# Kernel optimization log

Measured on AMD Instinct MI355X. Metric: run time of the kernel, lower is better.

Reference implementation:

```python
import jax, jax.numpy as jnp
import numpy as np

# hyperparameters (from init_kwargs / repo defaults)
AMP_COEF = 1.0
ARG_COEF = 1.0
SSIM_COEF = 1.0
BETA = 1.0
STFT_COEF = 1e-4
EPS = 1e-8
STFT_F = 12
STFT_S = 4


def _gauss_kernel(size=11, sigma=1.5):
    x = jnp.arange(size, dtype=jnp.float32) - (size - 1) / 2.0
    g = jnp.exp(-0.5 * (x / sigma) ** 2)
    k = jnp.outer(g, g)
    return k / jnp.sum(k)


def _depthwise_filter(img, k):
    # img: [B,H,W,C]; 11x11 gaussian, VALID padding, depthwise (per-channel)
    c = img.shape[-1]
    kern = jnp.tile(k[:, :, None, None], (1, 1, 1, c))  # HWIO, I=1, O=C
    return jax.lax.conv_general_dilated(
        img, kern, (1, 1), 'VALID',
        dimension_numbers=('NHWC', 'HWIO', 'NHWC'),
        feature_group_count=c)


def ssim(x, y, max_val=1.0):
    # faithful to tf.image.ssim defaults: filter 11, sigma 1.5, k1=0.01, k2=0.03
    c1 = (0.01 * max_val) ** 2
    c2 = (0.03 * max_val) ** 2
    k = _gauss_kernel()
    mu_x = _depthwise_filter(x, k)
    mu_y = _depthwise_filter(y, k)
    var_x = _depthwise_filter(x * x, k) - mu_x * mu_x
    var_y = _depthwise_filter(y * y, k) - mu_y * mu_y
    cov = _depthwise_filter(x * y, k) - mu_x * mu_y
    lum = (2.0 * mu_x * mu_y + c1) / (mu_x * mu_x + mu_y * mu_y + c1)
    cs = (2.0 * cov + c2) / (var_x + var_y + c2)
    return jnp.mean(lum * cs, axis=(1, 2, 3))  # [B]


def stft(image, f=STFT_F, s=STFT_S):
    # image: [B,N,N,C] -> batched patchwise 2D FFT, cropped to [:f//2,:f//2]
    n = image.shape[1]
    p = (n - f) // s + 1          # num_conv per axis
    half = f // 2
    rows = (jnp.arange(p) * s)[:, None] + jnp.arange(f)   # [P, f]
    patches = image[:, rows]                              # [B,P,f,N,C]
    patches = patches[:, :, :, rows]                      # [B,P,f,P,f,C]
    patches = jnp.transpose(patches, (0, 1, 3, 2, 4, 5))  # [B,Pi,Pj,f,f,C]
    b, c = image.shape[0], image.shape[-1]
    patches = patches.reshape(b, p * p, f, f, c)          # k = i*P + j ordering
    fft = jnp.fft.fft2(patches.astype(jnp.complex64), axes=(2, 3))
    return fft[:, :, :half, :half, :]                     # [B,P*P,half,half,C]


def _freq_filter(f=STFT_F):
    lin = jnp.linspace(0.0, 1.0, f // 2)[:, None]
    return (lin * lin.T)[:, :, None]                      # [half,half,1]


def setup_inputs() -> dict:
    key = jax.random.key(0)
    k1, k2, k3, k4 = jax.random.split(key, 4)
    B, N, C, L = 32, 160, 3, 128
    return {
        'mean': jax.random.normal(k1, (B, L), dtype=jnp.float32),
        'logvar': jax.random.normal(k2, (B, L), dtype=jnp.float32),
        'x_in': jax.random.uniform(k3, (B, N, N, C), dtype=jnp.float32),
        'x_out': jax.random.uniform(k4, (B, N, N, C), dtype=jnp.float32),
    }


def reference(mean, logvar, x_in, x_out):
    # KLD per sample
    var = jnp.exp(logvar)
    kld = -0.5 * jnp.sum(1.0 + logvar - var - mean * mean, axis=1)  # [B]
    # SSIM recon term
    recons = SSIM_COEF * ssim(x_in, x_out, 1.0)                     # [B]
    # patchwise STFT amp/phase loss ('ours')
    stft_out = stft(x_out, STFT_F, STFT_S)
    stft_in = stft(x_in, STFT_F, STFT_S)
    ff = _freq_filter(STFT_F)                                       # [half,half,1]
    arg_diff = jnp.abs(jnp.angle(stft_out + EPS) - jnp.angle(stft_in + EPS))
    amp_diff = jnp.abs(jnp.abs(stft_out) - jnp.abs(stft_in))
    arg_loss = jnp.sum(arg_diff * ff, axis=(1, 2, 3, 4))            # [B]
    amp_loss = jnp.sum(amp_diff * ff, axis=(1, 2, 3, 4))            # [B]
    stft_loss = ARG_COEF * arg_loss + AMP_COEF * amp_loss
    loss = jnp.mean(BETA * kld + recons + STFT_COEF * stft_loss)
    return loss
```

## Files before the change

kernel.cpp:

```cpp
#include <hip/hip_runtime.h>
#include <hip/hip_fp16.h>
#include <math.h>

#define BATCH 32
#define NPIX 160
#define LDIM 128
#define OUT_SZ 150

#define THREADS 512
#define N_BLOCKS 1825
#define SCRATCH_OFF 2880
#define VSTRIDE 1296
#define SMEM_FLOATS 9360

__device__ constexpr float TWC[12] = { 1.f, 0.86602540f, 0.5f, 0.f, -0.5f, -0.86602540f,
                                      -1.f,-0.86602540f,-0.5f, 0.f,  0.5f,  0.86602540f};
__device__ constexpr float TWS[12] = { 0.f,-0.5f,-0.86602540f,-1.f,-0.86602540f,-0.5f,
                                       0.f, 0.5f, 0.86602540f, 1.f, 0.86602540f, 0.5f};

__device__ constexpr float GW[11] = {0.00102838f, 0.00759876f, 0.03600076f, 0.10936070f,
                                     0.21300554f, 0.26601172f, 0.21300554f, 0.10936070f,
                                     0.03600076f, 0.00759876f, 0.00102838f};

__device__ __forceinline__ float fast_atan2f(float y, float x) {
    float ax = fabsf(x), ay = fabsf(y);
    float mx = fmaxf(ax, ay), mn = fminf(ax, ay);
    float z = mn / mx;
    float z2 = z * z;
    float p = fmaf(z2, -0.01172120f, 0.05265332f);
    p = fmaf(z2, p, -0.11643287f);
    p = fmaf(z2, p, 0.19354346f);
    p = fmaf(z2, p, -0.33262347f);
    p = fmaf(z2, p, 0.99997726f);
    p = p * z;
    if (ay > ax) p = 1.57079632679489662f - p;
    if (x < 0.f) p = 3.14159265358979323f - p;
    return (y < 0.f) ? -p : p;
}

__device__ __forceinline__ float4 extract_c(float4 f0, float4 f1, float4 f2, int c) {
    if (c == 0) return make_float4(f0.x, f0.w, f1.z, f2.y);
    if (c == 1) return make_float4(f0.y, f1.x, f1.w, f2.z);
    return make_float4(f0.z, f1.y, f2.x, f2.w);
}

__global__ __launch_bounds__(THREADS) void work_kernel(const float* __restrict__ xin,
                                                       const float* __restrict__ xout,
                                                       const float* __restrict__ mean,
                                                       const float* __restrict__ logvar,
                                                       float* __restrict__ out) {
    __shared__ __align__(16) float SMEM[SMEM_FLOATS];
    __shared__ float sm8[8];
    const int tid = threadIdx.x;
    const int gid = blockIdx.x;
    float acc = 0.f;

    if (gid == 1824) {
        float a = 0.f;
        for (int i = tid; i < BATCH * LDIM; i += THREADS) {
            float m = mean[i], lv = logvar[i];
            a += -0.5f * (1.f + lv - expf(lv) - m * m) * (1.f / 32.f);
        }
        #pragma unroll
        for (int o = 32; o > 0; o >>= 1) a += __shfl_down(a, o, 64);
        if ((tid & 63) == 0) sm8[tid >> 6] = a;
        __syncthreads();
        if (tid == 0) {
            float s = sm8[0];
            #pragma unroll
            for (int i = 1; i < 8; ++i) s += sm8[i];
            atomicAdd(out, s);
        }
        return;
    }

    int b    = gid / 57;
    int rem  = gid % 57;
    int c    = rem / 19;
    int tile = rem % 19;
    int r0 = tile * 8;
    __half2* HXY = (__half2*)SMEM;
    __half2* RD  = (__half2*)(SMEM + SCRATCH_OFF);

    for (int t = tid; t < 720; t += THREADS) {
        int rr = t / 40;
        int cq = t % 40;
        int row = r0 + rr;
        float4 xa = make_float4(0.f, 0.f, 0.f, 0.f);
        float4 xb = make_float4(0.f, 0.f, 0.f, 0.f);
        if (row < NPIX) {
            size_t off = ((size_t)(b * 160 + row) * 160 + cq * 4) * 3;
            const float4* qa = (const float4*)(xin + off);
            const float4* qb = (const float4*)(xout + off);
            float4 a0 = qa[0], a1 = qa[1], a2 = qa[2];
            float4 b0 = qb[0], b1 = qb[1], b2 = qb[2];
            xa = extract_c(a0, a1, a2, c);
            xb = extract_c(b0, b1, b2, c);
        }
        __half2 h[4] __attribute__((aligned(16)));
        h[0] = __floats2half2_rn(xa.x, xb.x);
        h[1] = __floats2half2_rn(xa.y, xb.y);
        h[2] = __floats2half2_rn(xa.z, xb.z);
        h[3] = __floats2half2_rn(xa.w, xb.w);
        *(float4*)&HXY[rr * 160 + cq * 4] = *(float4*)h;
    }
    __syncthreads();

    for (int t = tid; t < 608; t += THREADS) {
        int pc = t % 38;
        int r  = t / 38;
        float4 raw[3];
        raw[0] = *(const float4*)&HXY[r * 160 + pc * 4];
        raw[1] = *(const float4*)&HXY[r * 160 + pc * 4 + 4];
        raw[2] = *(const float4*)&HXY[r * 160 + pc * 4 + 8];
        const __half2* hp = (const __half2*)raw;
        float xa[12], xb[12];
        #pragma unroll
        for (int j = 0; j < 12; ++j) {
            float2 xy = __half22float2(hp[j]);
            xa[j] = xy.x; xb[j] = xy.y;
        }
        #pragma unroll
        for (int img = 0; img < 2; ++img) {
            const float* x = img ? xb : xa;
            float ev[5] = {x[1]+x[11], x[2]+x[10], x[3]+x[9], x[4]+x[8], x[5]+x[7]};
            float ov[5] = {x[1]-x[11], x[2]-x[10], x[3]-x[9], x[4]-x[8], x[5]-x[7]};
            #pragma unroll
            for (int vv = 0; vv < 5; ++vv) {
                int v = vv + 1;
                float re = x[0] + ((v & 1) ? -x[6] : x[6]);
                float im = 0.f;
                #pragma unroll
                for (int j = 1; j <= 5; ++j) {
                    int kk = (v * j) % 12;
                    re = fmaf(ev[j-1], TWC[kk], re);
                    im = fmaf(ov[j-1], TWS[kk], im);
                }
                RD[((r * 5 + vv) * 2 + img) * 38 + pc] = __floats2half2_rn(re, im);
            }
        }
    }
    __syncthreads();

    if (tid < 380) {
        int pc = tid % 38;
        int vv = (tid / 38) % 5;
        int g  = tid / 190;
        float FR0[5] = {0,0,0,0,0}, FI0[5] = {0,0,0,0,0};
        float FR1[5] = {0,0,0,0,0}, FI1[5] = {0,0,0,0,0};
        #pragma unroll
        for (int i = 0; i < 6; ++i) {
            int rlo = 4 * g + i, rhi = rlo + 6;
            float2 a0 = __half22float2(RD[((rlo * 5 + vv) * 2 + 0) * 38 + pc]);
            float2 a6 = __half22float2(RD[((rhi * 5 + vv) * 2 + 0) * 38 + pc]);
            float2 b0 = __half22float2(RD[((rlo * 5 + vv) * 2 + 1) * 38 + pc]);
            float2 b6 = __half22float2(RD[((rhi * 5 + vv) * 2 + 1) * 38 + pc]);
            float spR0 = a0.x + a6.x, spI0 = a0.y + a6.y;
            float smR0 = a0.x - a6.x, smI0 = a0.y - a6.y;
            float spR1 = b0.x + b6.x, spI1 = b0.y + b6.y;
            float smR1 = b0.x - b6.x, smI1 = b0.y - b6.y;
            #pragma unroll
            for (int uu = 0; uu < 5; ++uu) {
                int u = uu + 1;
                int kk = (u * i) % 12;
                float cu = TWC[kk], su = TWS[kk];
                float sR0 = (u & 1) ? smR0 : spR0, sI0 = (u & 1) ? smI0 : spI0;
                float sR1 = (u & 1) ? smR1 : spR1, sI1 = (u & 1) ? smI1 : spI1;
                FR0[uu] = fmaf(cu, sR0, fmaf(-su, sI0, FR0[uu]));
                FI0[uu] = fmaf(cu, sI0, fmaf( su, sR0, FI0[uu]));
                FR1[uu] = fmaf(cu, sR1, fmaf(-su, sI1, FR1[uu]));
                FI1[uu] = fmaf(cu, sI1, fmaf( su, sR1, FI1[uu]));
            }
        }
        float sacc = 0.f;
        #pragma unroll
        for (int uu = 0; uu < 5; ++uu) {
            float aI = fast_atan2f(FI0[uu], FR0[uu] + 1e-8f);
            float aO = fast_atan2f(FI1[uu], FR1[uu] + 1e-8f);
            float mI = sqrtf(FR0[uu] * FR0[uu] + FI0[uu] * FI0[uu]);
            float mO = sqrtf(FR1[uu] * FR1[uu] + FI1[uu] * FI1[uu]);
            float ff = (float)((uu + 1) * (vv + 1)) * 0.04f;
            sacc += ff * (fabsf(aO - aI) + fabsf(mO - mI));
        }
        acc += sacc * (1e-4f / 32.f);
    }
    __syncthreads();

    for (int t = tid; t < 320; t += THREADS) {
        int orow = t / 40;
        int cbase = (t % 40) * 4;
        float ax[4] = {0,0,0,0}, ay[4] = {0,0,0,0};
        float axx[4] = {0,0,0,0}, ayy[4] = {0,0,0,0}, axy[4] = {0,0,0,0};
        #pragma unroll
        for (int kk = 0; kk < 11; ++kk) {
            float4 raw = *(const float4*)&HXY[(orow + kk) * 160 + cbase];
            const __half2* hp = (const __half2*)&raw;
            float wg = GW[kk];
            #pragma unroll
            for (int o = 0; o < 4; ++o) {
                float2 xy = __half22float2(hp[o]);
                ax[o]  += wg * xy.x;          ay[o]  += wg * xy.y;
                axx[o] += wg * (xy.x * xy.x); ayy[o] += wg * (xy.y * xy.y);
                axy[o] += wg * (xy.x * xy.y);
            }
        }
        int base = SCRATCH_OFF + orow * 160 + cbase;
        *(float4*)&SMEM[base + 0 * VSTRIDE] = make_float4(ax[0],  ax[1],  ax[2],  ax[3]);
        *(float4*)&SMEM[base + 1 * VSTRIDE] = make_float4(ay[0],  ay[1],  ay[2],  ay[3]);
        *(float4*)&SMEM[base + 2 * VSTRIDE] = make_float4(axx[0], axx[1], axx[2], axx[3]);
        *(float4*)&SMEM[base + 3 * VSTRIDE] = make_float4(ayy[0], ayy[1], ayy[2], ayy[3]);
        *(float4*)&SMEM[base + 4 * VSTRIDE] = make_float4(axy[0], axy[1], axy[2], axy[3]);
    }
    __syncthreads();

    {
        float hacc = 0.f;
        for (int t = tid; t < 600; t += THREADS) {
            int orow = t / 75;
            int oc = (t % 75) * 2;
            float st[5][2];
            #pragma unroll
            for (int p = 0; p < 5; ++p) {
                float vals[12];
                #pragma unroll
                for (int kk = 0; kk < 12; ++kk)
                    vals[kk] = SMEM[SCRATCH_OFF + p * VSTRIDE + orow * 160 + oc + kk];
                float s0 = 0.f, s1 = 0.f;
                #pragma unroll
                for (int kk = 0; kk < 11; ++kk) {
                    s0 += GW[kk] * vals[kk];
                    s1 += GW[kk] * vals[kk + 1];
                }
                st[p][0] = s0; st[p][1] = s1;
            }
            const float c1 = 1e-4f, c2 = 9e-4f;
            if (r0 + orow < OUT_SZ) {
                #pragma unroll
                for (int o = 0; o < 2; ++o) {
                    float mx = st[0][o], my = st[1][o];
                    float vx = st[2][o] - mx * mx;
                    float vy = st[3][o] - my * my;
                    float cv = st[4][o] - mx * my;
                    float lum = (2.f * mx * my + c1) / (mx * mx + my * my + c1);
                    float cs  = (2.f * cv + c2) / (vx + vy + c2);
                    hacc += lum * cs;
                }
            }
        }
        acc += hacc * (1.f / (32.f * 150.f * 150.f * 3.f));
    }

    #pragma unroll
    for (int o = 32; o > 0; o >>= 1) acc += __shfl_down(acc, o, 64);
    if ((tid & 63) == 0) sm8[tid >> 6] = acc;
    __syncthreads();
    if (tid == 0) {
        float s = sm8[0];
        #pragma unroll
        for (int i = 1; i < 8; ++i) s += sm8[i];
        atomicAdd(out, s);
    }
}

extern "C" void kernel_launch(void* const* d_in, const int* in_sizes, int n_in,
                              void* d_out, int out_size, void* d_ws, size_t ws_size,
                              hipStream_t stream) {
    const float* mean   = (const float*)d_in[0];
    const float* logvar = (const float*)d_in[1];
    const float* xin    = (const float*)d_in[2];
    const float* xout   = (const float*)d_in[3];
    float* out = (float*)d_out;

    hipMemsetAsync(out, 0, sizeof(float), stream);
    work_kernel<<<N_BLOCKS, THREADS, 0, stream>>>(xin, xout, mean, logvar, out);
}
```

Measured before the change: 122.6 us.

## Use packed half2 math for STFT and SSIM filters, fast rcp/sqrt

Moves the row/column DFT and the SSIM separable Gaussian filtering from fp32 to packed __half2 arithmetic, so x and y channels are processed together in one instruction. The intermediate scratch layout shrinks: mu and E[x^2] are stored as half2 and only the cross term stays fp32, with padded row strides. Divisions become hardware reciprocal and sqrt builtins. This cuts ALU and LDS traffic, but fp16 accumulation of variance and FFT terms risks precision loss, especially in the SSIM variance subtraction.

```diff
diff --git a/kernel.cpp b/kernel.cpp
--- a/kernel.cpp
+++ b/kernel.cpp
@@ -9,9 +9,12 @@
 
 #define THREADS 512
 #define N_BLOCKS 1825
-#define SCRATCH_OFF 2880
-#define VSTRIDE 1296
-#define SMEM_FLOATS 9360
+#define RD_OFF   2880
+#define VPMU_OFF 2880
+#define VPVV_OFF 4192
+#define VPXY_OFF 5504
+#define VROWSTR  164
+#define SMEM_FLOATS 8960
 
 __device__ constexpr float TWC[12] = { 1.f, 0.86602540f, 0.5f, 0.f, -0.5f, -0.86602540f,
                                       -1.f,-0.86602540f,-0.5f, 0.f,  0.5f,  0.86602540f};
@@ -25,7 +28,7 @@
 __device__ __forceinline__ float fast_atan2f(float y, float x) {
     float ax = fabsf(x), ay = fabsf(y);
     float mx = fmaxf(ax, ay), mn = fminf(ax, ay);
-    float z = mn / mx;
+    float z = mn * __builtin_amdgcn_rcpf(mx);
     float z2 = z * z;
     float p = fmaf(z2, -0.01172120f, 0.05265332f);
     p = fmaf(z2, p, -0.11643287f);
@@ -38,6 +41,15 @@
     return (y < 0.f) ? -p : p;
 }
 
+__device__ __forceinline__ __half2 h2swap(__half2 v) {
+    unsigned u;
+    __builtin_memcpy(&u, &v, 4);
+    u = (u >> 16) | (u << 16);
+    __half2 r;
+    __builtin_memcpy(&r, &u, 4);
+    return r;
+}
+
 __device__ __forceinline__ float4 extract_c(float4 f0, float4 f1, float4 f2, int c) {
     if (c == 0) return make_float4(f0.x, f0.w, f1.z, f2.y);
     if (c == 1) return make_float4(f0.y, f1.x, f1.w, f2.z);
@@ -80,7 +92,8 @@
     int tile = rem % 19;
     int r0 = tile * 8;
     __half2* HXY = (__half2*)SMEM;
-    __half2* RD  = (__half2*)(SMEM + SCRATCH_OFF);
+    __half2* RD  = (__half2*)(SMEM + RD_OFF);
+    const __half2 hz = __float2half2_rn(0.f);
 
     for (int t = tid; t < 720; t += THREADS) {
         int rr = t / 40;
@@ -113,31 +126,28 @@
         raw[0] = *(const float4*)&HXY[r * 160 + pc * 4];
         raw[1] = *(const float4*)&HXY[r * 160 + pc * 4 + 4];
         raw[2] = *(const float4*)&HXY[r * 160 + pc * 4 + 8];
-        const __half2* hp = (const __half2*)raw;
-        float xa[12], xb[12];
-        #pragma unroll
-        for (int j = 0; j < 12; ++j) {
-            float2 xy = __half22float2(hp[j]);
-            xa[j] = xy.x; xb[j] = xy.y;
-        }
-        #pragma unroll
-        for (int img = 0; img < 2; ++img) {
-            const float* x = img ? xb : xa;
-            float ev[5] = {x[1]+x[11], x[2]+x[10], x[3]+x[9], x[4]+x[8], x[5]+x[7]};
-            float ov[5] = {x[1]-x[11], x[2]-x[10], x[3]-x[9], x[4]-x[8], x[5]-x[7]};
-            #pragma unroll
-            for (int vv = 0; vv < 5; ++vv) {
-                int v = vv + 1;
-                float re = x[0] + ((v & 1) ? -x[6] : x[6]);
-                float im = 0.f;
-                #pragma unroll
-                for (int j = 1; j <= 5; ++j) {
-                    int kk = (v * j) % 12;
-                    re = fmaf(ev[j-1], TWC[kk], re);
-                    im = fmaf(ov[j-1], TWS[kk], im);
-                }
-                RD[((r * 5 + vv) * 2 + img) * 38 + pc] = __floats2half2_rn(re, im);
-            }
+        const __half2* x = (const __half2*)raw;
+        __half2 ev[5], ov[5];
+        #pragma unroll
+        for (int j = 1; j <= 5; ++j) {
+            ev[j-1] = __hadd2(x[j], x[12 - j]);
+            ov[j-1] = __hsub2(x[j], x[12 - j]);
+        }
+        #pragma unroll
+        for (int vv = 0; vv < 5; ++vv) {
+            const int v = vv + 1;
+            __half2 re = (v & 1) ? __hsub2(x[0], x[6]) : __hadd2(x[0], x[6]);
+            __half2 im = hz;
+            #pragma unroll
+            for (int j = 1; j <= 5; ++j) {
+                const int kk = (v * j) % 12;
+                re = __hfma2(ev[j-1], __float2half2_rn(TWC[kk]), re);
+                im = __hfma2(ov[j-1], __float2half2_rn(TWS[kk]), im);
+            }
+            __half2 w2[2] __attribute__((aligned(8)));
+            w2[0] = re;
+            w2[1] = im;
+            *(float2*)&RD[((r * 5 + vv) * 38 + pc) * 2] = *(float2*)w2;
         }
     }
     __syncthreads();
@@ -146,39 +156,39 @@
         int pc = tid % 38;
         int vv = (tid / 38) % 5;
         int g  = tid / 190;
-        float FR0[5] = {0,0,0,0,0}, FI0[5] = {0,0,0,0,0};
-        float FR1[5] = {0,0,0,0,0}, FI1[5] = {0,0,0,0,0};
+        __half2 FR[5], FI[5];
+        #pragma unroll
+        for (int uu = 0; uu < 5; ++uu) { FR[uu] = hz; FI[uu] = hz; }
         #pragma unroll
         for (int i = 0; i < 6; ++i) {
             int rlo = 4 * g + i, rhi = rlo + 6;
-            float2 a0 = __half22float2(RD[((rlo * 5 + vv) * 2 + 0) * 38 + pc]);
-            float2 a6 = __half22float2(RD[((rhi * 5 + vv) * 2 + 0) * 38 + pc]);
-            float2 b0 = __half22float2(RD[((rlo * 5 + vv) * 2 + 1) * 38 + pc]);
-            float2 b6 = __half22float2(RD[((rhi * 5 + vv) * 2 + 1) * 38 + pc]);
-            float spR0 = a0.x + a6.x, spI0 = a0.y + a6.y;
-            float smR0 = a0.x - a6.x, smI0 = a0.y - a6.y;
-            float spR1 = b0.x + b6.x, spI1 = b0.y + b6.y;
-            float smR1 = b0.x - b6.x, smI1 = b0.y - b6.y;
+            __half2 lo[2] __attribute__((aligned(8)));
+            __half2 hi[2] __attribute__((aligned(8)));
+            *(float2*)lo = *(const float2*)&RD[((rlo * 5 + vv) * 38 + pc) * 2];
+            *(float2*)hi = *(const float2*)&RD[((rhi * 5 + vv) * 38 + pc) * 2];
+            __half2 spR = __hadd2(lo[0], hi[0]), smR = __hsub2(lo[0], hi[0]);
+            __half2 spI = __hadd2(lo[1], hi[1]), smI = __hsub2(lo[1], hi[1]);
             #pragma unroll
             for (int uu = 0; uu < 5; ++uu) {
-                int u = uu + 1;
-                int kk = (u * i) % 12;
-                float cu = TWC[kk], su = TWS[kk];
-                float sR0 = (u & 1) ? smR0 : spR0, sI0 = (u & 1) ? smI0 : spI0;
-                float sR1 = (u & 1) ? smR1 : spR1, sI1 = (u & 1) ? smI1 : spI1;
-                FR0[uu] = fmaf(cu, sR0, fmaf(-su, sI0, FR0[uu]));
-                FI0[uu] = fmaf(cu, sI0, fmaf( su, sR0, FI0[uu]));
-                FR1[uu] = fmaf(cu, sR1, fmaf(-su, sI1, FR1[uu]));
-                FI1[uu] = fmaf(cu, sI1, fmaf( su, sR1, FI1[uu]));
+                const int u = uu + 1;
+                const int kk = (u * i) % 12;
+                __half2 sR = (u & 1) ? smR : spR;
+                __half2 sI = (u & 1) ? smI : spI;
+                FR[uu] = __hfma2(sR, __float2half2_rn(TWC[kk]),
+                         __hfma2(sI, __float2half2_rn(-TWS[kk]), FR[uu]));
+                FI[uu] = __hfma2(sI, __float2half2_rn(TWC[kk]),
+                         __hfma2(sR, __float2half2_rn(TWS[kk]), FI[uu]));
             }
         }
         float sacc = 0.f;
         #pragma unroll
         for (int uu = 0; uu < 5; ++uu) {
-            float aI = fast_atan2f(FI0[uu], FR0[uu] + 1e-8f);
-            float aO = fast_atan2f(FI1[uu], FR1[uu] + 1e-8f);
-            float mI = sqrtf(FR0[uu] * FR0[uu] + FI0[uu] * FI0[uu]);
-            float mO = sqrtf(FR1[uu] * FR1[uu] + FI1[uu] * FI1[uu]);
+            float2 fr = __half22float2(FR[uu]);
+            float2 fi = __half22float2(FI[uu]);
+            float aI = fast_atan2f(fi.x, fr.x + 1e-8f);
+            float aO = fast_atan2f(fi.y, fr.y + 1e-8f);
+            float mI = __builtin_amdgcn_sqrtf(fmaf(fr.x, fr.x, fi.x * fi.x));
+            float mO = __builtin_amdgcn_sqrtf(fmaf(fr.y, fr.y, fi.y * fi.y));
             float ff = (float)((uu + 1) * (vv + 1)) * 0.04f;
             sacc += ff * (fabsf(aO - aI) + fabsf(mO - mI));
         }
@@ -189,27 +199,28 @@
     for (int t = tid; t < 320; t += THREADS) {
         int orow = t / 40;
         int cbase = (t % 40) * 4;
-        float ax[4] = {0,0,0,0}, ay[4] = {0,0,0,0};
-        float axx[4] = {0,0,0,0}, ayy[4] = {0,0,0,0}, axy[4] = {0,0,0,0};
+        __half2 amu[4], avv[4], axy[4];
+        #pragma unroll
+        for (int o = 0; o < 4; ++o) { amu[o] = hz; avv[o] = hz; axy[o] = hz; }
         #pragma unroll
         for (int kk = 0; kk < 11; ++kk) {
             float4 raw = *(const float4*)&HXY[(orow + kk) * 160 + cbase];
-            const __half2* hp = (const __half2*)&raw;
-            float wg = GW[kk];
+            const __half2* h = (const __half2*)&raw;
+            const __half2 w2 = __float2half2_rn(GW[kk]);
             #pragma unroll
             for (int o = 0; o < 4; ++o) {
-                float2 xy = __half22float2(hp[o]);
-                ax[o]  += wg * xy.x;          ay[o]  += wg * xy.y;
-                axx[o] += wg * (xy.x * xy.x); ayy[o] += wg * (xy.y * xy.y);
-                axy[o] += wg * (xy.x * xy.y);
-            }
-        }
-        int base = SCRATCH_OFF + orow * 160 + cbase;
-        *(float4*)&SMEM[base + 0 * VSTRIDE] = make_float4(ax[0],  ax[1],  ax[2],  ax[3]);
-        *(float4*)&SMEM[base + 1 * VSTRIDE] = make_float4(ay[0],  ay[1],  ay[2],  ay[3]);
-        *(float4*)&SMEM[base + 2 * VSTRIDE] = make_float4(axx[0], axx[1], axx[2], axx[3]);
-        *(float4*)&SMEM[base + 3 * VSTRIDE] = make_float4(ayy[0], ayy[1], ayy[2], ayy[3]);
-        *(float4*)&SMEM[base + 4 * VSTRIDE] = make_float4(axy[0], axy[1], axy[2], axy[3]);
+                __half2 t2 = __hmul2(w2, h[o]);
+                amu[o] = __hadd2(amu[o], t2);
+                avv[o] = __hfma2(t2, h[o], avv[o]);
+                axy[o] = __hfma2(t2, h2swap(h[o]), axy[o]);
+            }
+        }
+        int base = orow * VROWSTR + cbase;
+        *(float4*)&SMEM[VPMU_OFF + base] = *(float4*)amu;
+        *(float4*)&SMEM[VPVV_OFF + base] = *(float4*)avv;
+        *(float4*)&SMEM[VPXY_OFF + base] = make_float4(
+            __low2float(axy[0]), __low2float(axy[1]),
+            __low2float(axy[2]), __low2float(axy[3]));
     }
     __syncthreads();
 
@@ -218,31 +229,56 @@
         for (int t = tid; t < 600; t += THREADS) {
             int orow = t / 75;
             int oc = (t % 75) * 2;
-            float st[5][2];
-            #pragma unroll
-            for (int p = 0; p < 5; ++p) {
-                float vals[12];
-                #pragma unroll
-                for (int kk = 0; kk < 12; ++kk)
-                    vals[kk] = SMEM[SCRATCH_OFF + p * VSTRIDE + orow * 160 + oc + kk];
-                float s0 = 0.f, s1 = 0.f;
-                #pragma unroll
-                for (int kk = 0; kk < 11; ++kk) {
-                    s0 += GW[kk] * vals[kk];
-                    s1 += GW[kk] * vals[kk + 1];
-                }
-                st[p][0] = s0; st[p][1] = s1;
-            }
-            const float c1 = 1e-4f, c2 = 9e-4f;
+            int base = orow * VROWSTR + oc;
+            __half2 m[12], s0 = hz, s1 = hz;
+            #pragma unroll
+            for (int q = 0; q < 6; ++q)
+                *(float2*)&m[2 * q] = *(const float2*)&SMEM[VPMU_OFF + base + 2 * q];
+            #pragma unroll
+            for (int kk = 0; kk < 11; ++kk) {
+                const __half2 w2 = __float2half2_rn(GW[kk]);
+                s0 = __hfma2(w2, m[kk],     s0);
+                s1 = __hfma2(w2, m[kk + 1], s1);
+            }
+            float2 mu0 = __half22float2(s0);
+            float2 mu1 = __half22float2(s1);
+            __half2 v0 = hz, v1 = hz;
+            #pragma unroll
+            for (int q = 0; q < 6; ++q)
+                *(float2*)&m[2 * q] = *(const float2*)&SMEM[VPVV_OFF + base + 2 * q];
+            #pragma unroll
+            for (int kk = 0; kk < 11; ++kk) {
+                const __half2 w2 = __float2half2_rn(GW[kk]);
+                v0 = __hfma2(w2, m[kk],     v0);
+                v1 = __hfma2(w2, m[kk + 1], v1);
+            }
+            float2 vv0 = __half22float2(v0);
+            float2 vv1 = __half22float2(v1);
+            float zs[12];
+            #pragma unroll
+            for (int q = 0; q < 6; ++q) {
+                float2 y2 = *(const float2*)&SMEM[VPXY_OFF + base + 2 * q];
+                zs[2 * q] = y2.x; zs[2 * q + 1] = y2.y;
+            }
+            float xy0 = 0.f, xy1 = 0.f;
+            #pragma unroll
+            for (int kk = 0; kk < 11; ++kk) {
+                xy0 = fmaf(GW[kk], zs[kk],     xy0);
+                xy1 = fmaf(GW[kk], zs[kk + 1], xy1);
+            }
             if (r0 + orow < OUT_SZ) {
+                const float c1 = 1e-4f, c2 = 9e-4f;
                 #pragma unroll
                 for (int o = 0; o < 2; ++o) {
-                    float mx = st[0][o], my = st[1][o];
-                    float vx = st[2][o] - mx * mx;
-                    float vy = st[3][o] - my * my;
-                    float cv = st[4][o] - mx * my;
-                    float lum = (2.f * mx * my + c1) / (mx * mx + my * my + c1);
-                    float cs  = (2.f * cv + c2) / (vx + vy + c2);
+                    float mx = o ? mu1.x : mu0.x, my = o ? mu1.y : mu0.y;
+                    float ex = o ? vv1.x : vv0.x, ey = o ? vv1.y : vv0.y;
+                    float cv = (o ? xy1 : xy0) - mx * my;
+                    float vx = ex - mx * mx;
+                    float vy = ey - my * my;
+                    float lum = (2.f * mx * my + c1) *
+                                __builtin_amdgcn_rcpf(fmaf(mx, mx, my * my) + c1);
+                    float cs  = (2.f * cv + c2) *
+                                __builtin_amdgcn_rcpf(vx + vy + c2);
                     hacc += lum * cs;
                 }
             }
```

Result: faster. 105.2 us (-14.2%).
